# Optimization experiments

Measured on AMD Instinct MI355X. Metric: run time of the kernel, lower is better.

Reference implementation:

```python
import jax, jax.numpy as jnp
import numpy as np

HEADS = 16
DIM_HEAD = 64
EPS = 1e-8


def setup_inputs() -> dict:
    key = jax.random.key(0)
    ks = jax.random.split(key, 5)
    B, N, D = 2, 2048, 1024
    inner = HEADS * DIM_HEAD
    return {
        "x": jax.random.normal(ks[0], (B, N, D), jnp.float32),
        "Wq": jax.random.normal(ks[1], (D, inner), jnp.float32) * (D ** -0.5),
        "Wkv": jax.random.normal(ks[2], (D, 2 * inner), jnp.float32) * (D ** -0.5),
        "Wo": jax.random.normal(ks[3], (inner, D), jnp.float32) * (inner ** -0.5),
        "bo": jax.random.normal(ks[4], (D,), jnp.float32) * 0.02,
    }


def reference(x, Wq, Wkv, Wo, bo):
    # Self-attention (context = x), causal, memory-efficient path.
    # The chunked online-softmax in the source is mathematically equivalent to:
    #   gm = rowwise max of raw (unmasked) scores (stop-gradient, as in .detach())
    #   p  = exp(s - gm) with causal-masked entries zeroed (exp(-finfo.max) == 0)
    #   out = (p @ v) / (sum_j p + eps)
    B, N, D = x.shape
    H, Dh = HEADS, DIM_HEAD
    scale = Dh ** -0.5

    q = (x @ Wq).reshape(B, N, H, Dh).transpose(0, 2, 1, 3)  # b h n d
    kv = x @ Wkv
    k = kv[..., : H * Dh].reshape(B, N, H, Dh).transpose(0, 2, 1, 3)
    v = kv[..., H * Dh :].reshape(B, N, H, Dh).transpose(0, 2, 1, 3)

    s = jnp.einsum("bhid,bhjd->bhij", q * scale, k)  # b h i j
    gm = jax.lax.stop_gradient(jnp.max(s, axis=-1, keepdims=True))
    causal_mask = jnp.triu(jnp.ones((N, N), bool), 1)  # True above diagonal -> masked
    p = jnp.where(causal_mask, 0.0, jnp.exp(s - gm))
    num = jnp.einsum("bhij,bhjd->bhid", p, v)
    out = num / (jnp.sum(p, axis=-1, keepdims=True) + EPS)  # b h n d

    out = out.transpose(0, 2, 1, 3).reshape(B, N, H * Dh)  # b n (h d)
    return out @ Wo + bo
```

## Files before the change

### kernel.cpp

```cpp
#include <hip/hip_runtime.h>

typedef _Float16 f16;
typedef __attribute__((ext_vector_type(8))) _Float16 f16x8;
typedef __attribute__((ext_vector_type(4))) _Float16 f16x4;
typedef __attribute__((ext_vector_type(4))) float   f32x4;

typedef unsigned int u32;
typedef __attribute__((address_space(1))) const u32 gu32;
typedef __attribute__((address_space(3))) u32 lu32;

__device__ inline void gll16(const void* g, void* l) {
  __builtin_amdgcn_global_load_lds((gu32*)g, (lu32*)l, 16, 0, 0);
}

__global__ void cvt_f32_f16(const float* __restrict__ in, f16* __restrict__ out, int n4) {
  int i = blockIdx.x * blockDim.x + threadIdx.x;
  if (i < n4) {
    float4 v = ((const float4*)in)[i];
    f16x4 r = { (f16)v.x, (f16)v.y, (f16)v.z, (f16)v.w };
    ((f16x4*)out)[i] = r;
  }
}

__global__ void transpose3(const float* __restrict__ Wq, const float* __restrict__ Wkv,
                           const float* __restrict__ Wo, f16* __restrict__ WqkvT,
                           f16* __restrict__ WoT) {
  __shared__ float tile[32][33];
  int z = blockIdx.z;
  const float* src; f16* dst; int W;
  if (z == 0)      { src = Wq;  dst = WqkvT;                       W = 1024; }
  else if (z == 1) { src = Wkv; dst = WqkvT + (size_t)1024 * 1024; W = 2048; }
  else             { src = Wo;  dst = WoT;                         W = 1024; }
  int c0 = blockIdx.x * 32, r0 = blockIdx.y * 32;
  if (c0 >= W) return;
  int tx = threadIdx.x, ty = threadIdx.y;
  for (int i = 0; i < 4; i++)
    tile[ty + i * 8][tx] = src[(size_t)(r0 + ty + i * 8) * W + c0 + tx];
  __syncthreads();
  for (int i = 0; i < 4; i++)
    dst[(size_t)(c0 + ty + i * 8) * 1024 + r0 + tx] = (f16)tile[tx][ty + i * 8];
}

__global__ __launch_bounds__(256) void gemm1(
    const f16* __restrict__ A, const f16* __restrict__ Bt,
    f16* __restrict__ qb, f16* __restrict__ kb, f16* __restrict__ vtb) {
  const int K = 1024;
  __shared__ f16 As[128 * 32];
  __shared__ f16 Bs[128 * 32];
  int tid = threadIdx.x;
  int wave = tid >> 6, lane = tid & 63, quad = lane >> 4, l16 = lane & 15;
  int m0 = blockIdx.y * 128, n0 = blockIdx.x * 128;
  int wr = (wave >> 1) * 64, wc = (wave & 1) * 64;

  f32x4 acc[4][4] = {};

  int gA = (((lane & 3) ^ ((lane >> 3) & 3))) * 8;
  const f16* Ag = A  + (size_t)(m0 + wave * 32 + (lane >> 2)) * K + gA;
  const f16* Bg = Bt + (size_t)(n0 + wave * 32 + (lane >> 2)) * K + gA;
  f16* Asw = As + wave * 1024;
  f16* Bsw = Bs + wave * 1024;
  int rsz = (l16 >> 1) & 3;

  for (int k0 = 0; k0 < K; k0 += 32) {
    gll16(Ag + k0, Asw);
    gll16(Ag + (size_t)16 * K + k0, Asw + 512);
    gll16(Bg + k0, Bsw);
    gll16(Bg + (size_t)16 * K + k0, Bsw + 512);
    __syncthreads();
    f16x8 af[4], bf[4];
    for (int mt = 0; mt < 4; mt++)
      af[mt] = *(const f16x8*)&As[(wr + mt * 16 + l16) * 32 + ((quad ^ rsz) << 3)];
    for (int nt = 0; nt < 4; nt++)
      bf[nt] = *(const f16x8*)&Bs[(wc + nt * 16 + l16) * 32 + ((quad ^ rsz) << 3)];
    for (int mt = 0; mt < 4; mt++)
      for (int nt = 0; nt < 4; nt++)
        acc[mt][nt] = __builtin_amdgcn_mfma_f32_16x16x32_f16(af[mt], bf[nt], acc[mt][nt], 0, 0, 0);
    __syncthreads();
  }

  if (n0 < 2048) {
    for (int mt = 0; mt < 4; mt++)
      for (int nt = 0; nt < 4; nt++)
        for (int r = 0; r < 4; r++) {
          int row = m0 + wr + mt * 16 + quad * 4 + r;
          int col = n0 + wc + nt * 16 + l16;
          float v = acc[mt][nt][r];
          int b = row >> 11, n = row & 2047;
          if (col < 1024) {
            qb[(((size_t)b * 16 + (col >> 6)) * 2048 + n) * 64 + (col & 63)] =
                (f16)(v * 0.1803368801111137f);
          } else {
            int c = col - 1024;
            kb[(((size_t)b * 16 + (c >> 6)) * 2048 + n) * 64 + (c & 63)] = (f16)v;
          }
        }
  } else {
    for (int mt = 0; mt < 4; mt++)
      for (int nt = 0; nt < 4; nt++) {
        int rb = m0 + wr + mt * 16 + quad * 4;
        int c  = n0 + wc + nt * 16 + l16 - 2048;
        int b = rb >> 11, n = rb & 2047;
        f16x4 pk = { (f16)acc[mt][nt][0], (f16)acc[mt][nt][1],
                     (f16)acc[mt][nt][2], (f16)acc[mt][nt][3] };
        size_t idx = (((size_t)(b * 16 + (c >> 6)) * 32 + (n >> 6)) * 64 + (c & 63)) * 64 + (n & 63);
        *(f16x4*)&vtb[idx] = pk;
      }
  }
}

__global__ __launch_bounds__(256) void gemm2(
    const f16* __restrict__ A, const f16* __restrict__ Bt,
    const float* __restrict__ bo, float* __restrict__ outf) {
  const int K = 1024;
  __shared__ f16 As[128 * 32];
  __shared__ f16 Bs[64 * 32];
  int tid = threadIdx.x;
  int wave = tid >> 6, lane = tid & 63, quad = lane >> 4, l16 = lane & 15;
  int m0 = blockIdx.y * 128, n0 = blockIdx.x * 64;
  int wr = (wave >> 1) * 64, wc = (wave & 1) * 32;

  f32x4 acc[4][2] = {};

  int gA = (((lane & 3) ^ ((lane >> 3) & 3))) * 8;
  const f16* Ag = A  + (size_t)(m0 + wave * 32 + (lane >> 2)) * K + gA;
  const f16* Bg = Bt + (size_t)(n0 + wave * 16 + (lane >> 2)) * K + gA;
  f16* Asw = As + wave * 1024;
  f16* Bsw = Bs + wave * 512;
  int rsz = (l16 >> 1) & 3;

  for (int k0 = 0; k0 < K; k0 += 32) {
    gll16(Ag + k0, Asw);
    gll16(Ag + (size_t)16 * K + k0, Asw + 512);
    gll16(Bg + k0, Bsw);
    __syncthreads();
    f16x8 af[4], bf[2];
    for (int mt = 0; mt < 4; mt++)
      af[mt] = *(const f16x8*)&As[(wr + mt * 16 + l16) * 32 + ((quad ^ rsz) << 3)];
    for (int nt = 0; nt < 2; nt++)
      bf[nt] = *(const f16x8*)&Bs[(wc + nt * 16 + l16) * 32 + ((quad ^ rsz) << 3)];
    for (int mt = 0; mt < 4; mt++)
      for (int nt = 0; nt < 2; nt++)
        acc[mt][nt] = __builtin_amdgcn_mfma_f32_16x16x32_f16(af[mt], bf[nt], acc[mt][nt], 0, 0, 0);
    __syncthreads();
  }

  for (int mt = 0; mt < 4; mt++)
    for (int nt = 0; nt < 2; nt++)
      for (int r = 0; r < 4; r++) {
        int row = m0 + wr + mt * 16 + quad * 4 + r;
        int col = n0 + wc + nt * 16 + l16;
        outf[(size_t)row * 1024 + col] = acc[mt][nt][r] + bo[col];
      }
}

__global__ __launch_bounds__(256) void attn(
    const f16* __restrict__ qb, const f16* __restrict__ kb,
    const f16* __restrict__ vtb, f16* __restrict__ ob) {
  __shared__ f16 Ks[64 * 64];
  __shared__ f16 Vs[64 * 64];
  __shared__ f16 Ps[4][16 * 64];
  int tid = threadIdx.x, wave = tid >> 6, lane = tid & 63, quad = lane >> 4, l16 = lane & 15;
  int l7 = l16 & 7;

  int bx = blockIdx.x;
  int half = bx >> 8, r9 = bx & 255;
  int t = half ? 15 - (r9 & 15) : (r9 & 15);
  int bh = (half << 4) + (r9 >> 4);
  int qi0 = t * 128;
  int b = bh >> 4, h = bh & 15;

  const f16* Q  = qb  + (size_t)bh * 2048 * 64;
  const char* Kg = (const char*)(kb + (size_t)bh * 2048 * 64);
  const char* Vbase = (const char*)(vtb + (size_t)bh * 32 * 4096);
  int wq0 = qi0 + wave * 32;

  f16x8 qf[2][2];
  for (int mt = 0; mt < 2; mt++)
    for (int ks = 0; ks < 2; ks++)
      qf[mt][ks] = *(const f16x8*)&Q[(size_t)(wq0 + mt * 16 + l16) * 64 + ks * 32 + quad * 8];

  f32x4 acc[2][4] = {};
  float mrow[2] = { -1e30f, -1e30f }, lrow[2] = { 0.f, 0.f };

  int sg = ((lane & 7) ^ ((lane >> 3) & 7)) * 16;
  int jl = wave * 16 + (lane >> 3);

  for (int j0 = 0; j0 < qi0 + 128; j0 += 64) {
    const char* kg = Kg + (size_t)j0 * 128;
    const char* vt = Vbase + (size_t)(j0 >> 6) * 8192;
    gll16(kg + (size_t)jl * 128 + sg,        (char*)Ks + wave * 2048);
    gll16(kg + (size_t)(jl + 8) * 128 + sg,  (char*)Ks + wave * 2048 + 1024);
    gll16(vt + (size_t)jl * 128 + sg,        (char*)Vs + wave * 2048);
    gll16(vt + (size_t)(jl + 8) * 128 + sg,  (char*)Vs + wave * 2048 + 1024);
    __syncthreads();

    if (j0 <= wq0 + 31) {
      f16x8 kf[4][2], vf[4][2];
      for (int nt = 0; nt < 4; nt++)
        for (int ks = 0; ks < 2; ks++) {
          int pos = ((ks * 4 + quad) ^ l7) << 3;
          kf[nt][ks] = *(const f16x8*)&Ks[(nt * 16 + l16) * 64 + pos];
          vf[nt][ks] = *(const f16x8*)&Vs[(nt * 16 + l16) * 64 + pos];
        }

      for (int mt = 0; mt < 2; mt++) {
        int im = wq0 + mt * 16;
        if (j0 > im + 15) continue;
        int i = im + l16;

        f32x4 st[4];
        for (int nt = 0; nt < 4; nt++) {
          f32x4 z = {0.f, 0.f, 0.f, 0.f};
          z = __builtin_amdgcn_mfma_f32_16x16x32_f16(kf[nt][0], qf[mt][0], z, 0, 0, 0);
          z = __builtin_amdgcn_mfma_f32_16x16x32_f16(kf[nt][1], qf[mt][1], z, 0, 0, 0);
          st[nt] = z;
        }
        bool full = (j0 + 63 <= im);
        if (!full) {
          for (int nt = 0; nt < 4; nt++) {
            int jc = j0 + nt * 16 + quad * 4;
            for (int r = 0; r < 4; r++)
              st[nt][r] = (jc + r <= i) ? st[nt][r] : -1e30f;
          }
        }
        float v = fmaxf(fmaxf(fmaxf(st[0][0], st[0][1]), fmaxf(st[0][2], st[0][3])),
                        fmaxf(fmaxf(st[1][0], st[1][1]), fmaxf(st[1][2], st[1][3])));
        v = fmaxf(v, fmaxf(fmaxf(fmaxf(st[2][0], st[2][1]), fmaxf(st[2][2], st[2][3])),
                           fmaxf(fmaxf(st[3][0], st[3][1]), fmaxf(st[3][2], st[3][3]))));
        v = fmaxf(v, __shfl_xor(v, 16));
        v = fmaxf(v, __shfl_xor(v, 32));
        float mn = fmaxf(mrow[mt], v);
        float al = __builtin_amdgcn_exp2f(mrow[mt] - mn);
        mrow[mt] = mn;
        lrow[mt] *= al;
        for (int nt = 0; nt < 4; nt++)
          for (int r = 0; r < 4; r++) acc[mt][nt][r] *= al;

        float psum = 0.f;
        for (int nt = 0; nt < 4; nt++) {
          f16x4 pk;
          for (int r = 0; r < 4; r++) {
            float p = __builtin_amdgcn_exp2f(st[nt][r] - mn);
            psum += p;
            pk[r] = (f16)p;
          }
          int pos = (nt * 2 + (quad >> 1)) ^ l7;
          *(f16x4*)((char*)&Ps[wave][0] + l16 * 128 + pos * 16 + (quad & 1) * 8) = pk;
        }
        psum += __shfl_xor(psum, 16);
        psum += __shfl_xor(psum, 32);
        lrow[mt] += psum;

        for (int ks = 0; ks < 2; ks++) {
          f16x8 pf = *(const f16x8*)((char*)&Ps[wave][0] + l16 * 128 + (((ks * 4 + quad) ^ l7) * 16));
          for (int nt = 0; nt < 4; nt++)
            acc[mt][nt] = __builtin_amdgcn_mfma_f32_16x16x32_f16(vf[nt][ks], pf, acc[mt][nt], 0, 0, 0);
        }
      }
    }
    __syncthreads();
  }

  for (int mt = 0; mt < 2; mt++) {
    float inv = 1.f / (lrow[mt] + 1e-8f);
    int n = wq0 + mt * 16 + l16;
    for (int nt = 0; nt < 4; nt++) {
      f16x4 o = { (f16)(acc[mt][nt][0] * inv), (f16)(acc[mt][nt][1] * inv),
                  (f16)(acc[mt][nt][2] * inv), (f16)(acc[mt][nt][3] * inv) };
      *(f16x4*)&ob[((size_t)b * 2048 + n) * 1024 + h * 64 + nt * 16 + quad * 4] = o;
    }
  }
}

extern "C" void kernel_launch(void* const* d_in, const int* in_sizes, int n_in,
                              void* d_out, int out_size, void* d_ws, size_t ws_size,
                              hipStream_t stream) {
  const float* x   = (const float*)d_in[0];
  const float* Wq  = (const float*)d_in[1];
  const float* Wkv = (const float*)d_in[2];
  const float* Wo  = (const float*)d_in[3];
  const float* bo  = (const float*)d_in[4];
  float* out = (float*)d_out;

  char* ws = (char*)d_ws;
  f16* xb    = (f16*)ws;  ws += (size_t)4096 * 1024 * 2;
  f16* WqkvT = (f16*)ws;  ws += (size_t)3072 * 1024 * 2;
  f16* WoT   = (f16*)ws;  ws += (size_t)1024 * 1024 * 2;
  f16* qb    = (f16*)ws;  ws += (size_t)32 * 2048 * 64 * 2;
  f16* kb    = (f16*)ws;  ws += (size_t)32 * 2048 * 64 * 2;
  f16* vtb   = (f16*)ws;  ws += (size_t)32 * 64 * 2048 * 2;
  f16* ob    = xb;

  cvt_f32_f16<<<dim3(4096), 256, 0, stream>>>(x, xb, 4096 * 1024 / 4);
  transpose3<<<dim3(64, 32, 3), dim3(32, 8), 0, stream>>>(Wq, Wkv, Wo, WqkvT, WoT);

  gemm1<<<dim3(24, 32), 256, 0, stream>>>(xb, WqkvT, qb, kb, vtb);
  attn<<<dim3(512), 256, 0, stream>>>(qb, kb, vtb, ob);
  gemm2<<<dim3(16, 32), 256, 0, stream>>>(ob, WoT, bo, out);
}
```

Measured before the change: 197.3 us.

## Load K/V per wave into double-buffered registers, dropping shared-memory tiles

The attention kernel no longer stages K and V tiles in shared memory behind block-wide barriers. Each wave now loads its own K/V fragments straight from global memory into registers, double-buffered so the next tile's loads overlap the current tile's MFMA and softmax work. Block and wave indexing is remapped so each wave owns its own 32-row query tile with its own causal trip count. The online-softmax rescale is also skipped when no row max in the wave increases. In exchange, the four waves of a block each read K/V separately, so traffic through L2 rises, and the two register buffers raise VGPR pressure, which may lower occupancy.

```diff
diff --git a/kernel.cpp b/kernel.cpp
--- a/kernel.cpp
+++ b/kernel.cpp
@@ -156,23 +156,21 @@
 __global__ __launch_bounds__(256) void attn(
     const f16* __restrict__ qb, const f16* __restrict__ kb,
     const f16* __restrict__ vtb, f16* __restrict__ ob) {
-  __shared__ f16 Ks[64 * 64];
-  __shared__ f16 Vs[64 * 64];
   __shared__ f16 Ps[4][16 * 64];
   int tid = threadIdx.x, wave = tid >> 6, lane = tid & 63, quad = lane >> 4, l16 = lane & 15;
   int l7 = l16 & 7;
 
   int bx = blockIdx.x;
-  int half = bx >> 8, r9 = bx & 255;
-  int t = half ? 15 - (r9 & 15) : (r9 & 15);
-  int bh = (half << 4) + (r9 >> 4);
-  int qi0 = t * 128;
+  int half = bx >> 8, r = bx & 255;
+  int bh = ((r & 7) << 2) | ((r >> 3) & 3);
+  int s  = ((r >> 5) << 2) | wave;
+  int t  = half ? 63 - s : s;
+  int wq0 = t * 32;
   int b = bh >> 4, h = bh & 15;
 
   const f16* Q  = qb  + (size_t)bh * 2048 * 64;
-  const char* Kg = (const char*)(kb + (size_t)bh * 2048 * 64);
-  const char* Vbase = (const char*)(vtb + (size_t)bh * 32 * 4096);
-  int wq0 = qi0 + wave * 32;
+  const f16* Kg = kb  + (size_t)bh * 2048 * 64;
+  const f16* Vg = vtb + (size_t)bh * 32 * 4096;
 
   f16x8 qf[2][2];
   for (int mt = 0; mt < 2; mt++)
@@ -182,83 +180,88 @@
   f32x4 acc[2][4] = {};
   float mrow[2] = { -1e30f, -1e30f }, lrow[2] = { 0.f, 0.f };
 
-  int sg = ((lane & 7) ^ ((lane >> 3) & 7)) * 16;
-  int jl = wave * 16 + (lane >> 3);
-
-  for (int j0 = 0; j0 < qi0 + 128; j0 += 64) {
-    const char* kg = Kg + (size_t)j0 * 128;
-    const char* vt = Vbase + (size_t)(j0 >> 6) * 8192;
-    gll16(kg + (size_t)jl * 128 + sg,        (char*)Ks + wave * 2048);
-    gll16(kg + (size_t)(jl + 8) * 128 + sg,  (char*)Ks + wave * 2048 + 1024);
-    gll16(vt + (size_t)jl * 128 + sg,        (char*)Vs + wave * 2048);
-    gll16(vt + (size_t)(jl + 8) * 128 + sg,  (char*)Vs + wave * 2048 + 1024);
-    __syncthreads();
-
-    if (j0 <= wq0 + 31) {
-      f16x8 kf[4][2], vf[4][2];
-      for (int nt = 0; nt < 4; nt++)
-        for (int ks = 0; ks < 2; ks++) {
-          int pos = ((ks * 4 + quad) ^ l7) << 3;
-          kf[nt][ks] = *(const f16x8*)&Ks[(nt * 16 + l16) * 64 + pos];
-          vf[nt][ks] = *(const f16x8*)&Vs[(nt * 16 + l16) * 64 + pos];
+  int fragoff = (l16 * 64) + quad * 8;
+
+  auto loadKV = [&](f16x8 (&kf)[4][2], f16x8 (&vf)[4][2], int j0) {
+    const f16* kp = Kg + (size_t)j0 * 64;
+    const f16* vp = Vg + (size_t)(j0 >> 6) * 4096;
+    for (int nt = 0; nt < 4; nt++)
+      for (int ks = 0; ks < 2; ks++) {
+        int off = nt * 1024 + ks * 32 + fragoff;
+        kf[nt][ks] = *(const f16x8*)&kp[off];
+        vf[nt][ks] = *(const f16x8*)&vp[off];
+      }
+  };
+
+  auto compute = [&](const f16x8 (&kf)[4][2], const f16x8 (&vf)[4][2], int j0) {
+    for (int mt = 0; mt < 2; mt++) {
+      int im = wq0 + mt * 16;
+      int i  = im + l16;
+
+      f32x4 st[4];
+      for (int nt = 0; nt < 4; nt++) {
+        f32x4 z = {0.f, 0.f, 0.f, 0.f};
+        z = __builtin_amdgcn_mfma_f32_16x16x32_f16(kf[nt][0], qf[mt][0], z, 0, 0, 0);
+        z = __builtin_amdgcn_mfma_f32_16x16x32_f16(kf[nt][1], qf[mt][1], z, 0, 0, 0);
+        st[nt] = z;
+      }
+      if (j0 + 63 > im) {
+        for (int nt = 0; nt < 4; nt++) {
+          int jc = j0 + nt * 16 + quad * 4;
+          for (int rr = 0; rr < 4; rr++)
+            st[nt][rr] = (jc + rr <= i) ? st[nt][rr] : -1e30f;
         }
-
-      for (int mt = 0; mt < 2; mt++) {
-        int im = wq0 + mt * 16;
-        if (j0 > im + 15) continue;
-        int i = im + l16;
-
-        f32x4 st[4];
-        for (int nt = 0; nt < 4; nt++) {
-          f32x4 z = {0.f, 0.f, 0.f, 0.f};
-          z = __builtin_amdgcn_mfma_f32_16x16x32_f16(kf[nt][0], qf[mt][0], z, 0, 0, 0);
-          z = __builtin_amdgcn_mfma_f32_16x16x32_f16(kf[nt][1], qf[mt][1], z, 0, 0, 0);
-          st[nt] = z;
-        }
-        bool full = (j0 + 63 <= im);
-        if (!full) {
-          for (int nt = 0; nt < 4; nt++) {
-            int jc = j0 + nt * 16 + quad * 4;
-            for (int r = 0; r < 4; r++)
-              st[nt][r] = (jc + r <= i) ? st[nt][r] : -1e30f;
-          }
-        }
-        float v = fmaxf(fmaxf(fmaxf(st[0][0], st[0][1]), fmaxf(st[0][2], st[0][3])),
-                        fmaxf(fmaxf(st[1][0], st[1][1]), fmaxf(st[1][2], st[1][3])));
-        v = fmaxf(v, fmaxf(fmaxf(fmaxf(st[2][0], st[2][1]), fmaxf(st[2][2], st[2][3])),
-                           fmaxf(fmaxf(st[3][0], st[3][1]), fmaxf(st[3][2], st[3][3]))));
-        v = fmaxf(v, __shfl_xor(v, 16));
-        v = fmaxf(v, __shfl_xor(v, 32));
-        float mn = fmaxf(mrow[mt], v);
-        float al = __builtin_amdgcn_exp2f(mrow[mt] - mn);
-        mrow[mt] = mn;
+      }
+      float v = fmaxf(fmaxf(fmaxf(st[0][0], st[0][1]), fmaxf(st[0][2], st[0][3])),
+                      fmaxf(fmaxf(st[1][0], st[1][1]), fmaxf(st[1][2], st[1][3])));
+      v = fmaxf(v, fmaxf(fmaxf(fmaxf(st[2][0], st[2][1]), fmaxf(st[2][2], st[2][3])),
+                         fmaxf(fmaxf(st[3][0], st[3][1]), fmaxf(st[3][2], st[3][3]))));
+      v = fmaxf(v, __shfl_xor(v, 16));
+      v = fmaxf(v, __shfl_xor(v, 32));
+      float mold = mrow[mt];
+      float mn = fmaxf(mold, v);
+      mrow[mt] = mn;
+      if (__any(mn > mold)) {
+        float al = __builtin_amdgcn_exp2f(mold - mn);
         lrow[mt] *= al;
         for (int nt = 0; nt < 4; nt++)
-          for (int r = 0; r < 4; r++) acc[mt][nt][r] *= al;
-
-        float psum = 0.f;
-        for (int nt = 0; nt < 4; nt++) {
-          f16x4 pk;
-          for (int r = 0; r < 4; r++) {
-            float p = __builtin_amdgcn_exp2f(st[nt][r] - mn);
-            psum += p;
-            pk[r] = (f16)p;
-          }
-          int pos = (nt * 2 + (quad >> 1)) ^ l7;
-          *(f16x4*)((char*)&Ps[wave][0] + l16 * 128 + pos * 16 + (quad & 1) * 8) = pk;
+          for (int rr = 0; rr < 4; rr++) acc[mt][nt][rr] *= al;
+      }
+      float psum = 0.f;
+      for (int nt = 0; nt < 4; nt++) {
+        f16x4 pk;
+        for (int rr = 0; rr < 4; rr++) {
+          float p = __builtin_amdgcn_exp2f(st[nt][rr] - mn);
+          psum += p;
+          pk[rr] = (f16)p;
         }
-        psum += __shfl_xor(psum, 16);
-        psum += __shfl_xor(psum, 32);
-        lrow[mt] += psum;
-
-        for (int ks = 0; ks < 2; ks++) {
-          f16x8 pf = *(const f16x8*)((char*)&Ps[wave][0] + l16 * 128 + (((ks * 4 + quad) ^ l7) * 16));
-          for (int nt = 0; nt < 4; nt++)
-            acc[mt][nt] = __builtin_amdgcn_mfma_f32_16x16x32_f16(vf[nt][ks], pf, acc[mt][nt], 0, 0, 0);
-        }
+        int pos = (nt * 2 + (quad >> 1)) ^ l7;
+        *(f16x4*)((char*)&Ps[wave][0] + l16 * 128 + pos * 16 + (quad & 1) * 8) = pk;
+      }
+      psum += __shfl_xor(psum, 16);
+      psum += __shfl_xor(psum, 32);
+      lrow[mt] += psum;
+
+      for (int ks = 0; ks < 2; ks++) {
+        f16x8 pf = *(const f16x8*)((char*)&Ps[wave][0] + l16 * 128 + (((ks * 4 + quad) ^ l7) * 16));
+        for (int nt = 0; nt < 4; nt++)
+          acc[mt][nt] = __builtin_amdgcn_mfma_f32_16x16x32_f16(vf[nt][ks], pf, acc[mt][nt], 0, 0, 0);
       }
     }
-    __syncthreads();
+  };
+
+  int jend = wq0 + 32;
+  f16x8 kfA[4][2], vfA[4][2], kfB[4][2], vfB[4][2];
+  loadKV(kfA, vfA, 0);
+  for (int j0 = 0;;) {
+    if (j0 + 64 < jend) loadKV(kfB, vfB, j0 + 64);
+    compute(kfA, vfA, j0);
+    j0 += 64;
+    if (j0 >= jend) break;
+    if (j0 + 64 < jend) loadKV(kfA, vfA, j0 + 64);
+    compute(kfB, vfB, j0);
+    j0 += 64;
+    if (j0 >= jend) break;
   }
 
   for (int mt = 0; mt < 2; mt++) {
```

New measurement: 212.7 us. 1.08x slower.

## Shrink attention query tile to 64 rows, remap blocks per XCD, fuse prep kernels

Applied to the files above, without the earlier changes.

The attention kernel now gives each block 64 query rows (16 per wave) instead of 128, which doubles the grid to 1024 blocks. A new block-to-(head, tile) mapping groups heads by XCD and interleaves forward and reversed causal tiles to balance load. The kernel skips the accumulator rescale when no row max changed and adds launch_bounds occupancy 4. The f32-to-f16 conversion of x is folded into the weight-transpose kernel so one launch is dropped. In exchange, each loaded K/V tile is reused by fewer query rows, so K/V traffic per query row goes up.

```diff
diff --git a/kernel.cpp b/kernel.cpp
--- a/kernel.cpp
+++ b/kernel.cpp
@@ -13,27 +13,27 @@
   __builtin_amdgcn_global_load_lds((gu32*)g, (lu32*)l, 16, 0, 0);
 }
 
-__global__ void cvt_f32_f16(const float* __restrict__ in, f16* __restrict__ out, int n4) {
-  int i = blockIdx.x * blockDim.x + threadIdx.x;
-  if (i < n4) {
-    float4 v = ((const float4*)in)[i];
-    f16x4 r = { (f16)v.x, (f16)v.y, (f16)v.z, (f16)v.w };
-    ((f16x4*)out)[i] = r;
-  }
-}
-
-__global__ void transpose3(const float* __restrict__ Wq, const float* __restrict__ Wkv,
-                           const float* __restrict__ Wo, f16* __restrict__ WqkvT,
-                           f16* __restrict__ WoT) {
+__global__ void prep(const float* __restrict__ Wq, const float* __restrict__ Wkv,
+                     const float* __restrict__ Wo, const float* __restrict__ x,
+                     f16* __restrict__ WqkvT, f16* __restrict__ WoT, f16* __restrict__ xb) {
   __shared__ float tile[32][33];
   int z = blockIdx.z;
+  int tx = threadIdx.x, ty = threadIdx.y;
+  if (z == 3) {
+    size_t flat = ((size_t)(blockIdx.y * 64 + blockIdx.x) * 256 + ty * 32 + tx) * 2;
+    for (int i = 0; i < 2; i++) {
+      float4 v = ((const float4*)x)[flat + i];
+      f16x4 r = { (f16)v.x, (f16)v.y, (f16)v.z, (f16)v.w };
+      ((f16x4*)xb)[flat + i] = r;
+    }
+    return;
+  }
   const float* src; f16* dst; int W;
   if (z == 0)      { src = Wq;  dst = WqkvT;                       W = 1024; }
   else if (z == 1) { src = Wkv; dst = WqkvT + (size_t)1024 * 1024; W = 2048; }
   else             { src = Wo;  dst = WoT;                         W = 1024; }
   int c0 = blockIdx.x * 32, r0 = blockIdx.y * 32;
   if (c0 >= W) return;
-  int tx = threadIdx.x, ty = threadIdx.y;
   for (int i = 0; i < 4; i++)
     tile[ty + i * 8][tx] = src[(size_t)(r0 + ty + i * 8) * W + c0 + tx];
   __syncthreads();
@@ -153,7 +153,7 @@
       }
 }
 
-__global__ __launch_bounds__(256) void attn(
+__global__ __launch_bounds__(256, 4) void attn(
     const f16* __restrict__ qb, const f16* __restrict__ kb,
     const f16* __restrict__ vtb, f16* __restrict__ ob) {
   __shared__ f16 Ks[64 * 64];
@@ -163,29 +163,35 @@
   int l7 = l16 & 7;
 
   int bx = blockIdx.x;
-  int half = bx >> 8, r9 = bx & 255;
-  int t = half ? 15 - (r9 & 15) : (r9 & 15);
-  int bh = (half << 4) + (r9 >> 4);
-  int qi0 = t * 128;
+  int q = bx >> 8, r = bx & 255;
+  int xcd = r & 7, idx = r >> 3;
+  int bh = xcd * 4 + (idx & 3);
+  int srem = idx >> 2;
+  int t;
+  if (q == 0)      t = srem;
+  else if (q == 1) t = 15 - srem;
+  else if (q == 2) t = 16 + srem;
+  else             t = 31 - srem;
+  int qi0 = t * 64;
   int b = bh >> 4, h = bh & 15;
 
-  const f16* Q  = qb  + (size_t)bh * 2048 * 64;
+  const f16* Q  = qb + (size_t)bh * 2048 * 64;
   const char* Kg = (const char*)(kb + (size_t)bh * 2048 * 64);
   const char* Vbase = (const char*)(vtb + (size_t)bh * 32 * 4096);
-  int wq0 = qi0 + wave * 32;
-
-  f16x8 qf[2][2];
-  for (int mt = 0; mt < 2; mt++)
-    for (int ks = 0; ks < 2; ks++)
-      qf[mt][ks] = *(const f16x8*)&Q[(size_t)(wq0 + mt * 16 + l16) * 64 + ks * 32 + quad * 8];
-
-  f32x4 acc[2][4] = {};
-  float mrow[2] = { -1e30f, -1e30f }, lrow[2] = { 0.f, 0.f };
+  int wq0 = qi0 + wave * 16;
+  int i = wq0 + l16;
+
+  f16x8 qf[2];
+  for (int ks = 0; ks < 2; ks++)
+    qf[ks] = *(const f16x8*)&Q[(size_t)(wq0 + l16) * 64 + ks * 32 + quad * 8];
+
+  f32x4 acc[4] = {};
+  float mrow = -1e30f, lrow = 0.f;
 
   int sg = ((lane & 7) ^ ((lane >> 3) & 7)) * 16;
   int jl = wave * 16 + (lane >> 3);
 
-  for (int j0 = 0; j0 < qi0 + 128; j0 += 64) {
+  for (int j0 = 0; j0 < qi0 + 64; j0 += 64) {
     const char* kg = Kg + (size_t)j0 * 128;
     const char* vt = Vbase + (size_t)(j0 >> 6) * 8192;
     gll16(kg + (size_t)jl * 128 + sg,        (char*)Ks + wave * 2048);
@@ -194,7 +200,7 @@
     gll16(vt + (size_t)(jl + 8) * 128 + sg,  (char*)Vs + wave * 2048 + 1024);
     __syncthreads();
 
-    if (j0 <= wq0 + 31) {
+    if (j0 <= wq0 + 15) {
       f16x8 kf[4][2], vf[4][2];
       for (int nt = 0; nt < 4; nt++)
         for (int ks = 0; ks < 2; ks++) {
@@ -203,72 +209,65 @@
           vf[nt][ks] = *(const f16x8*)&Vs[(nt * 16 + l16) * 64 + pos];
         }
 
-      for (int mt = 0; mt < 2; mt++) {
-        int im = wq0 + mt * 16;
-        if (j0 > im + 15) continue;
-        int i = im + l16;
-
-        f32x4 st[4];
+      f32x4 st[4];
+      for (int nt = 0; nt < 4; nt++) {
+        f32x4 z = {0.f, 0.f, 0.f, 0.f};
+        z = __builtin_amdgcn_mfma_f32_16x16x32_f16(kf[nt][0], qf[0], z, 0, 0, 0);
+        z = __builtin_amdgcn_mfma_f32_16x16x32_f16(kf[nt][1], qf[1], z, 0, 0, 0);
+        st[nt] = z;
+      }
+      if (j0 + 63 > wq0) {
         for (int nt = 0; nt < 4; nt++) {
-          f32x4 z = {0.f, 0.f, 0.f, 0.f};
-          z = __builtin_amdgcn_mfma_f32_16x16x32_f16(kf[nt][0], qf[mt][0], z, 0, 0, 0);
-          z = __builtin_amdgcn_mfma_f32_16x16x32_f16(kf[nt][1], qf[mt][1], z, 0, 0, 0);
-          st[nt] = z;
-        }
-        bool full = (j0 + 63 <= im);
-        if (!full) {
-          for (int nt = 0; nt < 4; nt++) {
-            int jc = j0 + nt * 16 + quad * 4;
-            for (int r = 0; r < 4; r++)
-              st[nt][r] = (jc + r <= i) ? st[nt][r] : -1e30f;
-          }
-        }
-        float v = fmaxf(fmaxf(fmaxf(st[0][0], st[0][1]), fmaxf(st[0][2], st[0][3])),
-                        fmaxf(fmaxf(st[1][0], st[1][1]), fmaxf(st[1][2], st[1][3])));
-        v = fmaxf(v, fmaxf(fmaxf(fmaxf(st[2][0], st[2][1]), fmaxf(st[2][2], st[2][3])),
-                           fmaxf(fmaxf(st[3][0], st[3][1]), fmaxf(st[3][2], st[3][3]))));
-        v = fmaxf(v, __shfl_xor(v, 16));
-        v = fmaxf(v, __shfl_xor(v, 32));
-        float mn = fmaxf(mrow[mt], v);
-        float al = __builtin_amdgcn_exp2f(mrow[mt] - mn);
-        mrow[mt] = mn;
-        lrow[mt] *= al;
+          int jc = j0 + nt * 16 + quad * 4;
+          for (int rr = 0; rr < 4; rr++)
+            st[nt][rr] = (jc + rr <= i) ? st[nt][rr] : -1e30f;
+        }
+      }
+      float v = fmaxf(fmaxf(fmaxf(st[0][0], st[0][1]), fmaxf(st[0][2], st[0][3])),
+                      fmaxf(fmaxf(st[1][0], st[1][1]), fmaxf(st[1][2], st[1][3])));
+      v = fmaxf(v, fmaxf(fmaxf(fmaxf(st[2][0], st[2][1]), fmaxf(st[2][2], st[2][3])),
+                         fmaxf(fmaxf(st[3][0], st[3][1]), fmaxf(st[3][2], st[3][3]))));
+      v = fmaxf(v, __shfl_xor(v, 16));
+      v = fmaxf(v, __shfl_xor(v, 32));
+      float mold = mrow;
+      float mn = fmaxf(mold, v);
+      mrow = mn;
+      if (__any(mn > mold)) {
+        float al = __builtin_amdgcn_exp2f(mold - mn);
+        lrow *= al;
         for (int nt = 0; nt < 4; nt++)
-          for (int r = 0; r < 4; r++) acc[mt][nt][r] *= al;
-
-        float psum = 0.f;
-        for (int nt = 0; nt < 4; nt++) {
-          f16x4 pk;
-          for (int r = 0; r < 4; r++) {
-            float p = __builtin_amdgcn_exp2f(st[nt][r] - mn);
-            psum += p;
-            pk[r] = (f16)p;
-          }
-          int pos = (nt * 2 + (quad >> 1)) ^ l7;
-          *(f16x4*)((char*)&Ps[wave][0] + l16 * 128 + pos * 16 + (quad & 1) * 8) = pk;
-        }
-        psum += __shfl_xor(psum, 16);
-        psum += __shfl_xor(psum, 32);
-        lrow[mt] += psum;
-
-        for (int ks = 0; ks < 2; ks++) {
-          f16x8 pf = *(const f16x8*)((char*)&Ps[wave][0] + l16 * 128 + (((ks * 4 + quad) ^ l7) * 16));
-          for (int nt = 0; nt < 4; nt++)
-            acc[mt][nt] = __builtin_amdgcn_mfma_f32_16x16x32_f16(vf[nt][ks], pf, acc[mt][nt], 0, 0, 0);
-        }
+          for (int rr = 0; rr < 4; rr++) acc[nt][rr] *= al;
+      }
+      float psum = 0.f;
+      for (int nt = 0; nt < 4; nt++) {
+        f16x4 pk;
+        for (int rr = 0; rr < 4; rr++) {
+          float p = __builtin_amdgcn_exp2f(st[nt][rr] - mn);
+          psum += p;
+          pk[rr] = (f16)p;
+        }
+        int pos = (nt * 2 + (quad >> 1)) ^ l7;
+        *(f16x4*)((char*)&Ps[wave][0] + l16 * 128 + pos * 16 + (quad & 1) * 8) = pk;
+      }
+      psum += __shfl_xor(psum, 16);
+      psum += __shfl_xor(psum, 32);
+      lrow += psum;
+
+      for (int ks = 0; ks < 2; ks++) {
+        f16x8 pf = *(const f16x8*)((char*)&Ps[wave][0] + l16 * 128 + (((ks * 4 + quad) ^ l7) * 16));
+        for (int nt = 0; nt < 4; nt++)
+          acc[nt] = __builtin_amdgcn_mfma_f32_16x16x32_f16(vf[nt][ks], pf, acc[nt], 0, 0, 0);
       }
     }
     __syncthreads();
   }
 
-  for (int mt = 0; mt < 2; mt++) {
-    float inv = 1.f / (lrow[mt] + 1e-8f);
-    int n = wq0 + mt * 16 + l16;
-    for (int nt = 0; nt < 4; nt++) {
-      f16x4 o = { (f16)(acc[mt][nt][0] * inv), (f16)(acc[mt][nt][1] * inv),
-                  (f16)(acc[mt][nt][2] * inv), (f16)(acc[mt][nt][3] * inv) };
-      *(f16x4*)&ob[((size_t)b * 2048 + n) * 1024 + h * 64 + nt * 16 + quad * 4] = o;
-    }
+  float inv = 1.f / (lrow + 1e-8f);
+  int n = wq0 + l16;
+  for (int nt = 0; nt < 4; nt++) {
+    f16x4 o = { (f16)(acc[nt][0] * inv), (f16)(acc[nt][1] * inv),
+                (f16)(acc[nt][2] * inv), (f16)(acc[nt][3] * inv) };
+    *(f16x4*)&ob[((size_t)b * 2048 + n) * 1024 + h * 64 + nt * 16 + quad * 4] = o;
   }
 }
 
@@ -291,10 +290,8 @@
   f16* vtb   = (f16*)ws;  ws += (size_t)32 * 64 * 2048 * 2;
   f16* ob    = xb;
 
-  cvt_f32_f16<<<dim3(4096), 256, 0, stream>>>(x, xb, 4096 * 1024 / 4);
-  transpose3<<<dim3(64, 32, 3), dim3(32, 8), 0, stream>>>(Wq, Wkv, Wo, WqkvT, WoT);
-
+  prep<<<dim3(64, 32, 4), dim3(32, 8), 0, stream>>>(Wq, Wkv, Wo, x, WqkvT, WoT, xb);
   gemm1<<<dim3(24, 32), 256, 0, stream>>>(xb, WqkvT, qb, kb, vtb);
-  attn<<<dim3(512), 256, 0, stream>>>(qb, kb, vtb, ob);
+  attn<<<dim3(1024), 256, 0, stream>>>(qb, kb, vtb, ob);
   gemm2<<<dim3(16, 32), 256, 0, stream>>>(ob, WoT, bo, out);
 }
```

Result: faster. 180.4 us (-8.6%).
